# Performance work log

Measured on AMD Instinct MI355X. Metric: run time of the kernel, lower is better.

Reference implementation:

```python
import jax, jax.numpy as jnp
import numpy as np

N_A = 100000
N_B = 100000


def _mean_agg(x_src, src, dst, n_dst):
    # gather source features along edges, mean-aggregate into destination nodes
    msgs = x_src[src]                                        # [E, d]
    s = jax.ops.segment_sum(msgs, dst, num_segments=n_dst)   # [n_dst, d]
    ones = jnp.ones((dst.shape[0], 1), dtype=x_src.dtype)
    cnt = jax.ops.segment_sum(ones, dst, num_segments=n_dst)
    return s / jnp.maximum(cnt, jnp.asarray(1.0, x_src.dtype))


def setup_inputs() -> dict:
    key = jax.random.key(0)
    ks = jax.random.split(key, 13)
    E = 1200000
    d = 64
    return {
        "x_A": jax.random.normal(ks[0], (N_A, d), jnp.float32),
        "x_B": jax.random.normal(ks[1], (N_B, d), jnp.float32),
        "Wn": jax.random.normal(ks[2], (2, 3, d, d), jnp.float32) * 0.1,
        "Wr": jax.random.normal(ks[3], (2, 3, d, d), jnp.float32) * 0.1,
        "b": jax.random.normal(ks[4], (2, 3, d), jnp.float32) * 0.1,
        "W_out": jax.random.normal(ks[5], (d, d), jnp.float32) * 0.1,
        "b_out": jax.random.normal(ks[6], (d,), jnp.float32) * 0.1,
        "src0": jax.random.randint(ks[7], (E,), 0, N_A, jnp.int64 if jax.config.jax_enable_x64 else jnp.int32),
        "dst0": jax.random.randint(ks[8], (E,), 0, N_B, jnp.int32),
        "src1": jax.random.randint(ks[9], (E,), 0, N_B, jnp.int32),
        "dst1": jax.random.randint(ks[10], (E,), 0, N_A, jnp.int32),
        "src2": jax.random.randint(ks[11], (E,), 0, N_A, jnp.int32),
        "dst2": jax.random.randint(ks[12], (E,), 0, N_A, jnp.int32),
    }


def reference(x_A, x_B, Wn, Wr, b, W_out, b_out,
              src0, dst0, src1, dst1, src2, dst2):
    # Two stacked heterogeneous conv layers (SAGEConv-style per edge type,
    # summed across edge types per destination node type), then Linear+ReLU head.
    for l in range(2):
        m0 = _mean_agg(x_A, src0, dst0, N_B)  # A -> B
        m1 = _mean_agg(x_B, src1, dst1, N_A)  # B -> A
        m2 = _mean_agg(x_A, src2, dst2, N_A)  # A -> A
        new_B = m0 @ Wn[l, 0] + x_B @ Wr[l, 0] + b[l, 0]
        new_A = (m1 @ Wn[l, 1] + x_A @ Wr[l, 1] + b[l, 1]
                 + m2 @ Wn[l, 2] + x_A @ Wr[l, 2] + b[l, 2])
        x_A, x_B = new_A, new_B
    out_A = jax.nn.relu(x_A @ W_out + b_out)
    out_B = jax.nn.relu(x_B @ W_out + b_out)
    return jnp.concatenate([out_A, out_B], axis=0)  # [N_A + N_B, d]
```

## Files before the change

kernel.cpp:

```cpp
#include <hip/hip_runtime.h>
#include <hip/hip_bf16.h>

typedef __bf16 bf16_t;
typedef unsigned short u16;
typedef short short8 __attribute__((ext_vector_type(8)));
typedef float f32x4 __attribute__((ext_vector_type(4)));

#define BSHIFT 9
#define CAP 8192
#define TILE 8192

__device__ inline short f2bs(float v) {
    bf16_t h = (bf16_t)v;
    return __builtin_bit_cast(short, h);
}
__device__ inline float uif(unsigned u) { return __builtin_bit_cast(float, u); }

__global__ __launch_bounds__(256) void prep_convert(
    const float* __restrict__ xA, const float* __restrict__ xB,
    const float* __restrict__ Wn, const float* __restrict__ Wr,
    const float* __restrict__ Wout,
    u16* __restrict__ plane0, u16* __restrict__ wh, int NA, int NB) {
    int nA4 = NA * 16, nB4 = NB * 16;
    int bA = (nA4 + 255) / 256, bB = (nB4 + 255) / 256;
    int bi = blockIdx.x;
    int tid = threadIdx.x;
    if (bi < bA + bB) {
        const float* in = (bi < bA) ? xA : xB;
        u16* out = (bi < bA) ? plane0 : plane0 + (size_t)NA * 64;
        int i = (bi < bA ? bi : bi - bA) * 256 + tid;
        int n4 = (bi < bA) ? nA4 : nB4;
        if (i >= n4) return;
        float4 v = ((const float4*)in)[i];
        u16 o[4];
        o[0] = (u16)f2bs(v.x); o[1] = (u16)f2bs(v.y);
        o[2] = (u16)f2bs(v.z); o[3] = (u16)f2bs(v.w);
        *(uint2*)(out + (size_t)i * 4) = *(uint2*)o;
        return;
    }
    int mat = bi - bA - bB;
    u16* dstp = wh + (size_t)mat * 4096;
    for (int i = tid; i < 4096; i += 256) {
        int k = i >> 6, n = i & 63;
        float v;
        if (mat < 6) v = Wn[(size_t)mat * 4096 + i];
        else if (mat < 8) v = Wr[(size_t)((mat - 6) * 3 + 0) * 4096 + i];
        else if (mat < 10) v = Wr[(size_t)((mat - 8) * 3 + 1) * 4096 + i]
                             + Wr[(size_t)((mat - 8) * 3 + 2) * 4096 + i];
        else v = Wout[i];
        dstp[n * 64 + k] = (u16)f2bs(v);
    }
}

__global__ __launch_bounds__(256) void init_cursor(int* __restrict__ gcursor, int K) {
    int i = blockIdx.x * 256 + threadIdx.x;
    if (i < K) gcursor[i] = i * CAP;
}

__global__ __launch_bounds__(256) void partition_kernel(
    const int* __restrict__ s0, const int* __restrict__ d0,
    const int* __restrict__ s1, const int* __restrict__ d1,
    const int* __restrict__ s2, const int* __restrict__ d2,
    int* __restrict__ gcursor, int* __restrict__ pairs,
    int NB, int NA, int E, int total) {
    __shared__ int hist[1024];
    __shared__ int gbase[1024];
    __shared__ int ssum[256];
    __shared__ int2 buf[TILE];
    int tid = threadIdx.x;
    for (int tile = blockIdx.x * TILE; tile < total; tile += gridDim.x * TILE) {
        for (int i = tid; i < 1024; i += 256) hist[i] = 0;
        __syncthreads();
        int cnt = min(TILE, total - tile);
        int mybkt[32], mypk[32], myrank[32];
#pragma unroll
        for (int j = 0; j < 32; j++) {
            int idx = tile + j * 256 + tid;
            int g = -1, s = 0;
            if (idx < total) {
                if (idx < E) { s = s0[idx]; g = d0[idx]; }
                else if (idx < 2 * E) { s = s1[idx - E]; g = NB + d1[idx - E]; }
                else { s = s2[idx - 2 * E]; g = NB + NA + d2[idx - 2 * E]; }
            }
            if (g >= 0) {
                mybkt[j] = g >> BSHIFT;
                mypk[j] = ((g & ((1 << BSHIFT) - 1)) << 17) | s;
                myrank[j] = atomicAdd(&hist[mybkt[j]], 1);
            } else mybkt[j] = -1;
        }
        __syncthreads();
        int l[4]; int base4 = tid * 4; int ts = 0;
#pragma unroll
        for (int j = 0; j < 4; j++) { l[j] = hist[base4 + j]; ts += l[j]; }
        ssum[tid] = ts; __syncthreads();
        for (int off = 1; off < 256; off <<= 1) {
            int t = (tid >= off) ? ssum[tid - off] : 0; __syncthreads();
            ssum[tid] += t; __syncthreads();
        }
        int exc = tid ? ssum[tid - 1] : 0;
#pragma unroll
        for (int j = 0; j < 4; j++) {
            hist[base4 + j] = exc;
            if (l[j]) gbase[base4 + j] = atomicAdd(&gcursor[base4 + j], l[j]);
            exc += l[j];
        }
        __syncthreads();
#pragma unroll
        for (int j = 0; j < 32; j++) {
            if (mybkt[j] >= 0)
                buf[hist[mybkt[j]] + myrank[j]] = make_int2(mypk[j], mybkt[j]);
        }
        __syncthreads();
        for (int i = tid; i < cnt; i += 256) {
            int2 p = buf[i];
            pairs[gbase[p.y] + (i - hist[p.y])] = p.x;
        }
        __syncthreads();
    }
}

__global__ __launch_bounds__(256) void bucket_fill(const int* __restrict__ pairs,
                                                   const int* __restrict__ gcursor,
                                                   int* __restrict__ off_s,
                                                   int* __restrict__ off_e,
                                                   int* __restrict__ colidx, int M) {
    int b = blockIdx.x;
    int gb = b << BSHIFT;
    __shared__ int cnt[512], cur[512], ssum[256];
    int tid = threadIdx.x;
    int p0 = b * CAP, p1 = gcursor[b];
    for (int i = tid; i < 512; i += 256) cnt[i] = 0;
    __syncthreads();
    for (int e = p0 + tid; e < p1; e += 256)
        atomicAdd(&cnt[(unsigned)pairs[e] >> 17], 1);
    __syncthreads();
    int l0 = cnt[tid * 2], l1 = cnt[tid * 2 + 1];
    ssum[tid] = l0 + l1; __syncthreads();
    for (int o = 1; o < 256; o <<= 1) {
        int t = (tid >= o) ? ssum[tid - o] : 0; __syncthreads();
        ssum[tid] += t; __syncthreads();
    }
    int exc = tid ? ssum[tid - 1] : 0;
    cur[tid * 2] = exc;
    cur[tid * 2 + 1] = exc + l0;
    int g0 = gb + tid * 2, g1 = g0 + 1;
    if (g0 < M) { off_s[g0] = p0 + exc;      off_e[g0] = p0 + exc + l0; }
    if (g1 < M) { off_s[g1] = p0 + exc + l0; off_e[g1] = p0 + exc + l0 + l1; }
    __syncthreads();
    for (int e = p0 + tid; e < p1; e += 256) {
        int p = pairs[e];
        int pos = atomicAdd(&cur[(unsigned)p >> 17], 1);
        colidx[p0 + pos] = p & 0x1FFFF;
    }
}

__device__ __forceinline__ void acc8(uint4 u, f32x4& a0, f32x4& a1) {
    a0[0] += uif(u.x << 16); a0[1] += uif(u.x & 0xFFFF0000u);
    a0[2] += uif(u.y << 16); a0[3] += uif(u.y & 0xFFFF0000u);
    a1[0] += uif(u.z << 16); a1[1] += uif(u.z & 0xFFFF0000u);
    a1[2] += uif(u.w << 16); a1[3] += uif(u.w & 0xFFFF0000u);
}

__global__ __launch_bounds__(256) void gather_all(const u16* __restrict__ plane,
                                                  const int* __restrict__ colidx,
                                                  const int* __restrict__ off_s,
                                                  const int* __restrict__ off_e,
                                                  u16* __restrict__ meanB,
                                                  u16* __restrict__ meanA1,
                                                  u16* __restrict__ meanA2,
                                                  int NB, int NA) {
    int wid = (blockIdx.x * 256 + threadIdx.x) >> 6;
    int lane = threadIdx.x & 63;
    int oct = lane >> 3, fl = lane & 7;
    int M = NB + 2 * NA;
    int grow = wid * 8 + oct;
    if (grow >= M) return;

    const char* tab;
    u16* outp;
    int orow;
    if (grow < NB) { tab = (const char*)plane; outp = meanB; orow = grow; }
    else if (grow < NB + NA) { tab = (const char*)(plane + (size_t)NA * 64); outp = meanA1; orow = grow - NB; }
    else { tab = (const char*)plane; outp = meanA2; orow = grow - NB - NA; }

    int s0 = off_s[grow], s1 = off_e[grow];
    unsigned fo = (unsigned)(fl << 4);
    f32x4 a0 = {0.f, 0.f, 0.f, 0.f}, a1 = {0.f, 0.f, 0.f, 0.f};

    int e = s0;
    if (e + 3 < s1) {
        int c0 = colidx[e], c1 = colidx[e + 1];
        int c2 = colidx[e + 2], c3 = colidx[e + 3];
        while (e + 7 < s1) {
            uint4 u0 = *(const uint4*)(tab + (((unsigned)c0 << 7) | fo));
            uint4 u1 = *(const uint4*)(tab + (((unsigned)c1 << 7) | fo));
            uint4 u2 = *(const uint4*)(tab + (((unsigned)c2 << 7) | fo));
            uint4 u3 = *(const uint4*)(tab + (((unsigned)c3 << 7) | fo));
            c0 = colidx[e + 4]; c1 = colidx[e + 5];
            c2 = colidx[e + 6]; c3 = colidx[e + 7];
            acc8(u0, a0, a1); acc8(u1, a0, a1);
            acc8(u2, a0, a1); acc8(u3, a0, a1);
            e += 4;
        }
        {
            uint4 u0 = *(const uint4*)(tab + (((unsigned)c0 << 7) | fo));
            uint4 u1 = *(const uint4*)(tab + (((unsigned)c1 << 7) | fo));
            uint4 u2 = *(const uint4*)(tab + (((unsigned)c2 << 7) | fo));
            uint4 u3 = *(const uint4*)(tab + (((unsigned)c3 << 7) | fo));
            acc8(u0, a0, a1); acc8(u1, a0, a1);
            acc8(u2, a0, a1); acc8(u3, a0, a1);
            e += 4;
        }
    }
    for (; e < s1; ++e) {
        int c = colidx[e];
        uint4 u = *(const uint4*)(tab + (((unsigned)c << 7) | fo));
        acc8(u, a0, a1);
    }

    float inv = 1.0f / fmaxf((float)(s1 - s0), 1.0f);
    u16 o[8];
#pragma unroll
    for (int i = 0; i < 4; i++) o[i] = (u16)f2bs(a0[i] * inv);
#pragma unroll
    for (int i = 0; i < 4; i++) o[4 + i] = (u16)f2bs(a1[i] * inv);
    *(uint4*)(outp + (size_t)orow * 64 + fl * 8) = *(uint4*)o;
}

template <int NM, int RELU, int OUTF32>
__device__ __forceinline__ void lin_body(
    const u16* __restrict__ m0, const u16* __restrict__ m1,
    const u16* __restrict__ x,
    const u16* __restrict__ Wm0t, const u16* __restrict__ Wm1t,
    const u16* __restrict__ Wxt,
    const float* __restrict__ bias0, const float* __restrict__ bias1,
    void* __restrict__ outv, int nrows, int blk) {
    const int lane = threadIdx.x & 63;
    const int wave = threadIdx.x >> 6;
    const int row0 = blk * 64 + wave * 16;
    if (row0 >= nrows) return;
    const int r = lane & 15;
    const int q = lane >> 4;

    short8 wm0f[2][4], wm1f[2][4], wxf[2][4];
#pragma unroll
    for (int ks = 0; ks < 2; ks++) {
#pragma unroll
        for (int t = 0; t < 4; t++) {
            size_t widx = (size_t)(t * 16 + r) * 64 + ks * 32 + q * 8;
            if (NM >= 1) wm0f[ks][t] = *(const short8*)(Wm0t + widx);
            if (NM >= 2) wm1f[ks][t] = *(const short8*)(Wm1t + widx);
            wxf[ks][t] = *(const short8*)(Wxt + widx);
        }
    }

    f32x4 acc[4];
#pragma unroll
    for (int t = 0; t < 4; t++) {
        float bv = bias0[t * 16 + r];
        if (bias1) bv += bias1[t * 16 + r];
        acc[t][0] = bv; acc[t][1] = bv; acc[t][2] = bv; acc[t][3] = bv;
    }

    const int arow = row0 + r;
    const bool avalid = arow < nrows;
    short8 zf;
#pragma unroll
    for (int j = 0; j < 8; j++) zf[j] = 0;

    if (NM >= 1) {
#pragma unroll
        for (int ks = 0; ks < 2; ks++) {
            short8 af = avalid ? *(const short8*)(m0 + (size_t)arow * 64 + ks * 32 + q * 8) : zf;
#pragma unroll
            for (int t = 0; t < 4; t++)
                acc[t] = __builtin_amdgcn_mfma_f32_16x16x32_bf16(af, wm0f[ks][t], acc[t], 0, 0, 0);
        }
    }
    if (NM >= 2) {
#pragma unroll
        for (int ks = 0; ks < 2; ks++) {
            short8 af = avalid ? *(const short8*)(m1 + (size_t)arow * 64 + ks * 32 + q * 8) : zf;
#pragma unroll
            for (int t = 0; t < 4; t++)
                acc[t] = __builtin_amdgcn_mfma_f32_16x16x32_bf16(af, wm1f[ks][t], acc[t], 0, 0, 0);
        }
    }
#pragma unroll
    for (int ks = 0; ks < 2; ks++) {
        short8 xf = avalid ? *(const short8*)(x + (size_t)arow * 64 + ks * 32 + q * 8) : zf;
#pragma unroll
        for (int t = 0; t < 4; t++)
            acc[t] = __builtin_amdgcn_mfma_f32_16x16x32_bf16(xf, wxf[ks][t], acc[t], 0, 0, 0);
    }

#pragma unroll
    for (int t = 0; t < 4; t++) {
#pragma unroll
        for (int rr = 0; rr < 4; rr++) {
            int row = row0 + q * 4 + rr;
            if (row < nrows) {
                float v = acc[t][rr];
                if (RELU) v = fmaxf(v, 0.0f);
                if (OUTF32) ((float*)outv)[(size_t)row * 64 + t * 16 + r] = v;
                else ((u16*)outv)[(size_t)row * 64 + t * 16 + r] = (u16)f2bs(v);
            }
        }
    }
}

__global__ __launch_bounds__(256) void layer_kernel(
    const u16* __restrict__ plane_in, u16* __restrict__ plane_out,
    const u16* __restrict__ meanB, const u16* __restrict__ meanA1,
    const u16* __restrict__ meanA2, const u16* __restrict__ wh,
    const float* __restrict__ bvec, int l, int NA, int NB, int blocksB) {
    if ((int)blockIdx.x < blocksB) {
        lin_body<1, 0, 0>(meanB, nullptr, plane_in + (size_t)NA * 64,
                          wh + (size_t)(l * 3 + 0) * 4096, nullptr,
                          wh + (size_t)(6 + l) * 4096,
                          bvec + (size_t)(l * 3 + 0) * 64, nullptr,
                          plane_out + (size_t)NA * 64, NB, blockIdx.x);
    } else {
        lin_body<2, 0, 0>(meanA1, meanA2, plane_in,
                          wh + (size_t)(l * 3 + 1) * 4096, wh + (size_t)(l * 3 + 2) * 4096,
                          wh + (size_t)(8 + l) * 4096,
                          bvec + (size_t)(l * 3 + 1) * 64, bvec + (size_t)(l * 3 + 2) * 64,
                          plane_out, NA, blockIdx.x - blocksB);
    }
}

__global__ __launch_bounds__(256) void head_kernel(
    const u16* __restrict__ plane_in, const u16* __restrict__ wh,
    const float* __restrict__ b_out, float* __restrict__ out, int nrows) {
    lin_body<0, 1, 1>(nullptr, nullptr, plane_in,
                      nullptr, nullptr, wh + (size_t)10 * 4096,
                      b_out, nullptr, out, nrows, blockIdx.x);
}

extern "C" void kernel_launch(void* const* d_in, const int* in_sizes, int n_in,
                              void* d_out, int out_size, void* d_ws, size_t ws_size,
                              hipStream_t stream) {
    const float* xA_in = (const float*)d_in[0];
    const float* xB_in = (const float*)d_in[1];
    const float* Wn = (const float*)d_in[2];
    const float* Wr = (const float*)d_in[3];
    const float* b = (const float*)d_in[4];
    const float* W_out = (const float*)d_in[5];
    const float* b_out = (const float*)d_in[6];
    const int* src0 = (const int*)d_in[7];
    const int* dst0 = (const int*)d_in[8];
    const int* src1 = (const int*)d_in[9];
    const int* dst1 = (const int*)d_in[10];
    const int* src2 = (const int*)d_in[11];
    const int* dst2 = (const int*)d_in[12];

    const int NA = in_sizes[0] / 64;
    const int NB = in_sizes[1] / 64;
    const int E = in_sizes[7];
    const int M = NB + NA + NA;
    const int total = 3 * E;
    const int K = (M + (1 << BSHIFT) - 1) >> BSHIFT;

    const size_t PL = (size_t)(NA + NB) * 64;
    u16* plane[2];
    plane[0] = (u16*)d_ws;
    plane[1] = plane[0] + PL;
    u16* wh     = plane[1] + PL;
    u16* meanB  = wh + 11 * 4096;
    u16* meanA1 = meanB + (size_t)NB * 64;
    u16* meanA2 = meanA1 + (size_t)NA * 64;
    int* gcursor= (int*)(meanA2 + (size_t)NA * 64);
    int* off_s  = gcursor + 1024;
    int* off_e  = off_s + M;
    int* colidx = off_e + M;
    int* pairs  = (int*)meanB;

    int bA = (NA * 16 + 255) / 256, bB = (NB * 16 + 255) / 256;
    prep_convert<<<bA + bB + 11, 256, 0, stream>>>(
        xA_in, xB_in, Wn, Wr, W_out, plane[0], wh, NA, NB);

    init_cursor<<<(K + 255) / 256, 256, 0, stream>>>(gcursor, K);
    int ntiles = (total + TILE - 1) / TILE;
    partition_kernel<<<ntiles, 256, 0, stream>>>(src0, dst0, src1, dst1, src2, dst2,
                                                 gcursor, pairs, NB, NA, E, total);
    bucket_fill<<<K, 256, 0, stream>>>(pairs, gcursor, off_s, off_e, colidx, M);

    const int blocksB = (NB + 63) / 64;
    const int blocksA = (NA + 63) / 64;
    int p = 0;
    for (int l = 0; l < 2; l++) {
        gather_all<<<(M + 31) / 32, 256, 0, stream>>>(plane[p], colidx, off_s, off_e,
                                                      meanB, meanA1, meanA2, NB, NA);
        layer_kernel<<<blocksB + blocksA, 256, 0, stream>>>(
            plane[p], plane[1 - p], meanB, meanA1, meanA2, wh, b, l, NA, NB, blocksB);
        p = 1 - p;
    }

    head_kernel<<<(NA + NB + 63) / 64, 256, 0, stream>>>(
        plane[p], wh, b_out, (float*)d_out, NA + NB);
}
```

Baseline: 440.3 us.

## Simplify partition scatter and use wave-shuffle scan in bucket fill

The partition kernel drops the LDS staging buffer and block-wide prefix scan, scattering each edge directly to its global bucket slot via the reserved cursor plus its local rank, and halves the tile size to 4096. The bucket fill kernel moves to 512 threads (one per destination row) and replaces the barrier-heavy Hillis-Steele scan with a wavefront shuffle scan plus an 8-entry cross-wave combine. This removes many __syncthreads and LDS traffic, at the cost of less coalesced global writes in the partition scatter and roughly twice as many global atomics on the cursors.

```diff
diff --git a/kernel.cpp b/kernel.cpp
--- a/kernel.cpp
+++ b/kernel.cpp
@@ -8,7 +8,7 @@
 
 #define BSHIFT 9
 #define CAP 8192
-#define TILE 8192
+#define TILE 4096
 
 __device__ inline short f2bs(float v) {
     bf16_t h = (bf16_t)v;
@@ -65,16 +65,13 @@
     int NB, int NA, int E, int total) {
     __shared__ int hist[1024];
     __shared__ int gbase[1024];
-    __shared__ int ssum[256];
-    __shared__ int2 buf[TILE];
     int tid = threadIdx.x;
     for (int tile = blockIdx.x * TILE; tile < total; tile += gridDim.x * TILE) {
         for (int i = tid; i < 1024; i += 256) hist[i] = 0;
         __syncthreads();
-        int cnt = min(TILE, total - tile);
-        int mybkt[32], mypk[32], myrank[32];
-#pragma unroll
-        for (int j = 0; j < 32; j++) {
+        int mybkt[16], mypk[16], myrank[16];
+#pragma unroll
+        for (int j = 0; j < 16; j++) {
             int idx = tile + j * 256 + tid;
             int g = -1, s = 0;
             if (idx < total) {
@@ -89,65 +86,57 @@
             } else mybkt[j] = -1;
         }
         __syncthreads();
-        int l[4]; int base4 = tid * 4; int ts = 0;
-#pragma unroll
-        for (int j = 0; j < 4; j++) { l[j] = hist[base4 + j]; ts += l[j]; }
-        ssum[tid] = ts; __syncthreads();
-        for (int off = 1; off < 256; off <<= 1) {
-            int t = (tid >= off) ? ssum[tid - off] : 0; __syncthreads();
-            ssum[tid] += t; __syncthreads();
-        }
-        int exc = tid ? ssum[tid - 1] : 0;
-#pragma unroll
-        for (int j = 0; j < 4; j++) {
-            hist[base4 + j] = exc;
-            if (l[j]) gbase[base4 + j] = atomicAdd(&gcursor[base4 + j], l[j]);
-            exc += l[j];
+        for (int bq = tid; bq < 1024; bq += 256) {
+            int c = hist[bq];
+            if (c) gbase[bq] = atomicAdd(&gcursor[bq], c);
         }
         __syncthreads();
 #pragma unroll
-        for (int j = 0; j < 32; j++) {
+        for (int j = 0; j < 16; j++) {
             if (mybkt[j] >= 0)
-                buf[hist[mybkt[j]] + myrank[j]] = make_int2(mypk[j], mybkt[j]);
+                pairs[gbase[mybkt[j]] + myrank[j]] = mypk[j];
         }
         __syncthreads();
-        for (int i = tid; i < cnt; i += 256) {
-            int2 p = buf[i];
-            pairs[gbase[p.y] + (i - hist[p.y])] = p.x;
-        }
-        __syncthreads();
-    }
-}
-
-__global__ __launch_bounds__(256) void bucket_fill(const int* __restrict__ pairs,
+    }
+}
+
+__global__ __launch_bounds__(512) void bucket_fill(const int* __restrict__ pairs,
                                                    const int* __restrict__ gcursor,
                                                    int* __restrict__ off_s,
                                                    int* __restrict__ off_e,
                                                    int* __restrict__ colidx, int M) {
     int b = blockIdx.x;
     int gb = b << BSHIFT;
-    __shared__ int cnt[512], cur[512], ssum[256];
+    __shared__ int cnt[512], cur[512], wsum[8];
     int tid = threadIdx.x;
+    int lane = tid & 63, w = tid >> 6;
     int p0 = b * CAP, p1 = gcursor[b];
-    for (int i = tid; i < 512; i += 256) cnt[i] = 0;
-    __syncthreads();
-    for (int e = p0 + tid; e < p1; e += 256)
+    cnt[tid] = 0;
+    __syncthreads();
+    for (int e = p0 + tid; e < p1; e += 512)
         atomicAdd(&cnt[(unsigned)pairs[e] >> 17], 1);
     __syncthreads();
-    int l0 = cnt[tid * 2], l1 = cnt[tid * 2 + 1];
-    ssum[tid] = l0 + l1; __syncthreads();
-    for (int o = 1; o < 256; o <<= 1) {
-        int t = (tid >= o) ? ssum[tid - o] : 0; __syncthreads();
-        ssum[tid] += t; __syncthreads();
-    }
-    int exc = tid ? ssum[tid - 1] : 0;
-    cur[tid * 2] = exc;
-    cur[tid * 2 + 1] = exc + l0;
-    int g0 = gb + tid * 2, g1 = g0 + 1;
-    if (g0 < M) { off_s[g0] = p0 + exc;      off_e[g0] = p0 + exc + l0; }
-    if (g1 < M) { off_s[g1] = p0 + exc + l0; off_e[g1] = p0 + exc + l0 + l1; }
-    __syncthreads();
-    for (int e = p0 + tid; e < p1; e += 256) {
+    int v = cnt[tid];
+    int x = v;
+#pragma unroll
+    for (int off = 1; off < 64; off <<= 1) {
+        int n = __shfl_up(x, off);
+        if (lane >= off) x += n;
+    }
+    if (lane == 63) wsum[w] = x;
+    __syncthreads();
+    if (tid == 0) {
+        int s = 0;
+#pragma unroll
+        for (int i = 0; i < 8; i++) { int t = wsum[i]; wsum[i] = s; s += t; }
+    }
+    __syncthreads();
+    int excl = x - v + wsum[w];
+    cur[tid] = excl;
+    int g = gb + tid;
+    if (g < M) { off_s[g] = p0 + excl; off_e[g] = p0 + excl + v; }
+    __syncthreads();
+    for (int e = p0 + tid; e < p1; e += 512) {
         int p = pairs[e];
         int pos = atomicAdd(&cur[(unsigned)p >> 17], 1);
         colidx[p0 + pos] = p & 0x1FFFF;
@@ -383,7 +372,7 @@
     int ntiles = (total + TILE - 1) / TILE;
     partition_kernel<<<ntiles, 256, 0, stream>>>(src0, dst0, src1, dst1, src2, dst2,
                                                  gcursor, pairs, NB, NA, E, total);
-    bucket_fill<<<K, 256, 0, stream>>>(pairs, gcursor, off_s, off_e, colidx, M);
+    bucket_fill<<<K, 512, 0, stream>>>(pairs, gcursor, off_s, off_e, colidx, M);
 
     const int blocksB = (NB + 63) / 64;
     const int blocksA = (NA + 63) / 64;
```

New measurement: 427.2 us. -3.0%, faster.
